# Kernel tuning notes

Hardware: AMD Instinct MI355X
Metric: run time of the kernel (lower is better)

Reference implementation:

```python
import jax, jax.numpy as jnp
import numpy as np

B, D, L, H = 8, 512, 2048, 8
DH = D // H
NEG = -1e30


def setup_inputs() -> dict:
    key = jax.random.key(0)
    k1, k2, k3, k4 = jax.random.split(key, 4)
    queries = jax.random.normal(k1, (B, D, L), dtype=jnp.float32)
    mask = jax.random.randint(k2, (B, L), 0, 2, dtype=jnp.int32)
    w_mem = jax.random.normal(k3, (2 * D, D), dtype=jnp.float32) * (1.0 / np.sqrt(D))
    w_q = jax.random.normal(k4, (D, D), dtype=jnp.float32) * (1.0 / np.sqrt(D))
    return {"queries": queries, "mask": mask, "w_mem": w_mem, "w_q": w_q}


def reference(queries, mask, w_mem, w_q):
    # 1x1 conv == pointwise GEMM over channel dim. queries: [B, D, L]
    memory = jnp.einsum('od,bdl->blo', w_mem, queries)  # [B, L, 2D]
    query = jnp.einsum('od,bdl->blo', w_q, queries)     # [B, L, D]

    def split_heads(x):  # [B, L, C] -> [B, H, L, C/H]
        b, l, c = x.shape
        return x.reshape(b, l, H, c // H).transpose(0, 2, 1, 3)

    k, v = memory[..., :D], memory[..., D:]
    Q = split_heads(query) * (DH ** -0.5)  # [B, H, L, DH]
    K = split_heads(k)
    V = split_heads(v)

    logits = jnp.einsum('bhqd,bhkd->bhqk', Q, K)  # [B, H, L, L]
    m = mask.astype(jnp.float32)[:, None, None, :]  # [B, 1, 1, L]
    logits = logits * m + (1.0 - m) * NEG
    weights = jax.nn.softmax(logits, axis=-1)
    x = jnp.einsum('bhqk,bhkd->bhqd', weights, V)  # [B, H, L, DH]
    # combine heads -> [B, L, D] -> transpose back to [B, D, L]
    out = x.transpose(0, 2, 1, 3).reshape(B, L, D).transpose(0, 2, 1)
    return out
```

## Files before the change

kernel.cpp:

```cpp
#include <hip/hip_runtime.h>
#include <hip/hip_bf16.h>

#define NB 8
#define ND 512
#define NL 2048
#define NH 8
#define NDH 64
#define VROWS 72

typedef __attribute__((ext_vector_type(8))) short bf16x8;
typedef __attribute__((ext_vector_type(4))) float f32x4;
typedef __attribute__((ext_vector_type(4))) unsigned int u32x4;

__device__ __forceinline__ unsigned short f2bf(float x) {
    return (unsigned short)((__float_as_uint(x) + 0x8000u) >> 16);
}

__device__ __forceinline__ float exp2_fast(float x) {
#if __has_builtin(__builtin_amdgcn_exp2f)
    return __builtin_amdgcn_exp2f(x);
#else
    return exp2f(x);
#endif
}

__device__ __forceinline__ unsigned int pack_bf16(float a, float b) {
#if __has_builtin(__builtin_amdgcn_cvt_pk_bf16_f32)
    auto r = __builtin_amdgcn_cvt_pk_bf16_f32(a, b);
    unsigned int u;
    __builtin_memcpy(&u, &r, 4);
    return u;
#else
    unsigned int ua = __float_as_uint(a) + 0x8000u;
    unsigned int ub = __float_as_uint(b) + 0x8000u;
    return __builtin_amdgcn_perm(ub, ua, 0x07060302u);
#endif
}

__device__ __forceinline__ int perm64(int k) {
    return (k & 32) | ((k & 12) << 1) | ((k & 16) >> 2) | (k & 3);
}

__device__ __forceinline__ void async16(void* lds, const void* g) {
    __builtin_amdgcn_global_load_lds(
        (const __attribute__((address_space(1))) unsigned int*)g,
        (__attribute__((address_space(3))) unsigned int*)lds, 16, 0, 0);
}

__global__ __launch_bounds__(256) void prep(
    const float* __restrict__ qin,
    const float* __restrict__ w_mem, const float* __restrict__ w_q,
    const int* __restrict__ maskp,
    unsigned short* __restrict__ Xt, unsigned short* __restrict__ Wc,
    unsigned short* __restrict__ Vt, unsigned short* __restrict__ Kh,
    int* __restrict__ cmap, int* __restrict__ ntile)
{
    const int bid = blockIdx.x;
    const int t = threadIdx.x;
    if (bid < 2048) {
        __shared__ __align__(16) unsigned short T[64][72];
        const int l0 = (bid & 31) * 64, d0 = ((bid >> 5) & 7) * 64, b = bid >> 8;
        const float* X = qin + ((size_t)b * ND + d0) * NL + l0;
        #pragma unroll
        for (int i = 0; i < 4; ++i) {
            int e = t + i * 256;
            int d = e >> 4, l4 = (e & 15) * 4;
            float4 v = *(const float4*)(X + (size_t)d * NL + l4);
            T[l4 + 0][d] = f2bf(v.x);
            T[l4 + 1][d] = f2bf(v.y);
            T[l4 + 2][d] = f2bf(v.z);
            T[l4 + 3][d] = f2bf(v.w);
        }
        __syncthreads();
        #pragma unroll
        for (int i = 0; i < 2; ++i) {
            int e = t + i * 256;
            int row = e >> 3, c8 = (e & 7) * 8;
            *(bf16x8*)(Xt + ((size_t)b * NL + l0 + row) * ND + d0 + c8) =
                *(const bf16x8*)&T[row][c8];
        }
    } else if (bid < 2432) {
        int idx = ((bid - 2048) * 256 + t) * 8;
        int o = idx >> 9, k = idx & 511;
        const float* src;
        float sc;
        if (o < 1024) { src = w_mem + (size_t)o * ND + k; sc = 1.0f; }
        else          { src = w_q + (size_t)(o - 1024) * ND + k;
                        sc = 0.125f * 1.4426950408889634f; }
        float4 f0 = *(const float4*)src;
        float4 f1 = *(const float4*)(src + 4);
        ushort4 p0 = { f2bf(f0.x * sc), f2bf(f0.y * sc), f2bf(f0.z * sc), f2bf(f0.w * sc) };
        ushort4 p1 = { f2bf(f1.x * sc), f2bf(f1.y * sc), f2bf(f1.z * sc), f2bf(f1.w * sc) };
        *(ushort4*)(Wc + idx) = p0;
        *(ushort4*)(Wc + idx + 4) = p1;
    } else {
        __shared__ int wsum[4];
        const int b = bid - 2432;
        const int lane = t & 63, wv = t >> 6;
        int4 ma = *(const int4*)&maskp[b * NL + t * 8];
        int4 mb = *(const int4*)&maskp[b * NL + t * 8 + 4];
        int m[8] = {ma.x, ma.y, ma.z, ma.w, mb.x, mb.y, mb.z, mb.w};
        int loc = 0;
        #pragma unroll
        for (int i = 0; i < 8; ++i) loc += m[i];
        int sc = loc;
        #pragma unroll
        for (int off = 1; off < 64; off <<= 1) {
            int v = __shfl_up(sc, off);
            if (lane >= off) sc += v;
        }
        if (lane == 63) wsum[wv] = sc;
        __syncthreads();
        int wbase = 0;
        #pragma unroll
        for (int i = 0; i < 4; ++i) if (i < wv) wbase += wsum[i];
        int j = wbase + sc - loc;
        #pragma unroll
        for (int i = 0; i < 8; ++i) {
            cmap[b * NL + t * 8 + i] = m[i] ? j : -1;
            j += m[i];
        }
        const int nb = wsum[0] + wsum[1] + wsum[2] + wsum[3];
        const int Nt = (nb + 63) & ~63;
        if (t == 0) ntile[b] = Nt >> 6;
        const int pad = Nt - nb;
        for (int h = 0; h < NH; ++h) {
            unsigned short* row64 = Vt + (((size_t)(b * NH + h)) * VROWS + 64) * NL;
            for (int jj = t; jj < Nt; jj += 256)
                row64[(jj & ~63) | perm64(jj & 63)] =
                    (jj < nb) ? (unsigned short)0x3F80 : (unsigned short)0;
            for (int e = t; e < pad * 64; e += 256) {
                int jj = nb + (e >> 6), dd = e & 63;
                int slot = (jj & ~63) | perm64(jj & 63);
                Vt[(((size_t)(b * NH + h)) * VROWS + dd) * NL + slot] = 0;
                Kh[(((size_t)(b * NH + h)) * NL + jj) * NDH + dd] = 0;
            }
        }
    }
}

__global__ __launch_bounds__(256, 3) void proj_mfma(
    const unsigned short* __restrict__ Wc,
    const unsigned short* __restrict__ Xt,
    const int* __restrict__ cmap,
    unsigned short* __restrict__ Kh,
    unsigned short* __restrict__ Qh,
    unsigned short* __restrict__ Vt)
{
    __shared__ __align__(16) unsigned short As[128 * 64];
    __shared__ __align__(16) unsigned short Bs[128 * 64];

    const int b  = blockIdx.z;
    const int m0 = blockIdx.y * 128;
    const int n0 = blockIdx.x * 128;
    const int t  = threadIdx.x;
    const int w = t >> 6, lane = t & 63, quad = lane >> 4, lq = lane & 15;
    const int wo = (w >> 1) * 64, wl = (w & 1) * 64;
    const int lr = lane >> 3;
    const int cbsw = (lane & 7) ^ lr;
    const bool isV = (m0 >= 512) && (m0 < 1024);
    const f32x4 z4 = {0.f, 0.f, 0.f, 0.f};
    const int sw[2] = {(quad ^ (lq & 7)) * 8, ((4 + quad) ^ (lq & 7)) * 8};

    f32x4 acc[4][4];
    #pragma unroll
    for (int im = 0; im < 4; ++im)
        #pragma unroll
        for (int in = 0; in < 4; ++in) acc[im][in] = z4;

    if (!isV) {
        for (int k0 = 0; k0 < ND; k0 += 64) {
            __syncthreads();
            #pragma unroll 2
            for (int i = w; i < 32; i += 4) {
                if (i < 16) {
                    int R = i * 8;
                    async16(&As[R * 64],
                            Wc + (size_t)(m0 + R + lr) * ND + k0 + cbsw * 8);
                } else {
                    int R = (i - 16) * 8;
                    async16(&Bs[R * 64],
                            Xt + ((size_t)b * NL + n0 + R + lr) * ND + k0 + cbsw * 8);
                }
            }
            __syncthreads();
            #pragma unroll
            for (int ks = 0; ks < 2; ++ks) {
                bf16x8 af[4], bfr[4];
                #pragma unroll
                for (int im = 0; im < 4; ++im)
                    af[im] = *(const bf16x8*)&As[(wo + im * 16 + lq) * 64 + sw[ks]];
                #pragma unroll
                for (int in = 0; in < 4; ++in)
                    bfr[in] = *(const bf16x8*)&Bs[(wl + in * 16 + lq) * 64 + sw[ks]];
                #pragma unroll
                for (int im = 0; im < 4; ++im)
                    #pragma unroll
                    for (int in = 0; in < 4; ++in)
                        acc[im][in] = __builtin_amdgcn_mfma_f32_16x16x32_bf16(
                            af[im], bfr[in], acc[im][in], 0, 0, 0);
            }
        }
        if (m0 < 512) {
            int j[4];
            #pragma unroll
            for (int in = 0; in < 4; ++in)
                j[in] = cmap[b * NL + n0 + wl + in * 16 + lq];
            #pragma unroll
            for (int im = 0; im < 4; ++im) {
                int o  = (m0 + wo + im * 16 + quad * 4) & 511;
                int hh = o >> 6, dh = o & 63;
                #pragma unroll
                for (int in = 0; in < 4; ++in) {
                    if (j[in] >= 0) {
                        ushort4 pk = { f2bf(acc[im][in][0]), f2bf(acc[im][in][1]),
                                       f2bf(acc[im][in][2]), f2bf(acc[im][in][3]) };
                        *(ushort4*)&Kh[(((size_t)b * NH + hh) * NL + j[in]) * NDH + dh] = pk;
                    }
                }
            }
        } else {
            #pragma unroll
            for (int im = 0; im < 4; ++im) {
                int o  = (m0 + wo + im * 16 + quad * 4) & 511;
                int hh = o >> 6, dh = o & 63;
                #pragma unroll
                for (int in = 0; in < 4; ++in) {
                    int l = n0 + wl + in * 16 + lq;
                    ushort4 pk = { f2bf(acc[im][in][0]), f2bf(acc[im][in][1]),
                                   f2bf(acc[im][in][2]), f2bf(acc[im][in][3]) };
                    *(ushort4*)&Qh[(((size_t)b * NH + hh) * NL + l) * NDH + dh] = pk;
                }
            }
        }
    } else {
        for (int k0 = 0; k0 < ND; k0 += 64) {
            __syncthreads();
            #pragma unroll 2
            for (int i = w; i < 32; i += 4) {
                if (i < 16) {
                    int R = i * 8;
                    async16(&As[R * 64],
                            Wc + (size_t)(m0 + R + lr) * ND + k0 + cbsw * 8);
                } else {
                    int R = (i - 16) * 8;
                    async16(&Bs[R * 64],
                            Xt + ((size_t)b * NL + n0 + R + lr) * ND + k0 + cbsw * 8);
                }
            }
            __syncthreads();
            #pragma unroll
            for (int ks = 0; ks < 2; ++ks) {
                bf16x8 af[4], bfr[4];
                #pragma unroll
                for (int im = 0; im < 4; ++im)
                    af[im] = *(const bf16x8*)&As[(wo + im * 16 + lq) * 64 + sw[ks]];
                #pragma unroll
                for (int in = 0; in < 4; ++in)
                    bfr[in] = *(const bf16x8*)&Bs[(wl + in * 16 + lq) * 64 + sw[ks]];
                #pragma unroll
                for (int im = 0; im < 4; ++im)
                    #pragma unroll
                    for (int in = 0; in < 4; ++in)
                        acc[im][in] = __builtin_amdgcn_mfma_f32_16x16x32_bf16(
                            bfr[im], af[in], acc[im][in], 0, 0, 0);
            }
        }
        #pragma unroll
        for (int im = 0; im < 4; ++im) {
            int l4 = n0 + wl + im * 16 + quad * 4;
            int4 j4 = *(const int4*)&cmap[b * NL + l4];
            int jj[4] = {j4.x, j4.y, j4.z, j4.w};
            int slot[4];
            #pragma unroll
            for (int r = 0; r < 4; ++r)
                slot[r] = (jj[r] & ~63) | perm64(jj[r] & 63);
            #pragma unroll
            for (int in = 0; in < 4; ++in) {
                int o  = m0 - 512 + wo + in * 16 + lq;
                int hh = o >> 6, dd = o & 63;
                const size_t rowbase = (((size_t)(b * NH + hh)) * VROWS + dd) * NL;
                #pragma unroll
                for (int r = 0; r < 4; ++r)
                    if (jj[r] >= 0)
                        Vt[rowbase + slot[r]] = f2bf(acc[im][in][r]);
            }
        }
    }
}

__global__ __launch_bounds__(512, 4) void attn_mfma(
    const unsigned short* __restrict__ Qh,
    const unsigned short* __restrict__ Kh,
    const unsigned short* __restrict__ Vt,
    const int* __restrict__ ntilep,
    float* __restrict__ out)
{
    __shared__ __align__(16) unsigned short Ks2[2][64 * 64];
    __shared__ __align__(16) unsigned short Vs2[2][80 * 64];

    const int id = blockIdx.x;
    const int h  = id & 7;
    const int b  = (id >> 3) & 7;
    const int q0 = (id >> 6) * 256;
    const int t = threadIdx.x;
    const int w = t >> 6;
    const int lane = t & 63, quad = lane >> 4, lq = lane & 15;
    const int lr = lane >> 3;
    const int cbsw = (lane & 7) ^ lr;
    const f32x4 z4 = {0.f, 0.f, 0.f, 0.f};

    const unsigned short* Qg = Qh + ((size_t)(b * NH + h)) * NL * NDH;
    const unsigned short* Kg = Kh + ((size_t)(b * NH + h)) * NL * NDH;
    const unsigned short* Vg = Vt + ((size_t)(b * NH + h)) * VROWS * NL;
    const int ntiles = ntilep[b];

    const int sw0 = (quad ^ (lq & 7)) * 8;
    const int sw1 = ((4 + quad) ^ (lq & 7)) * 8;

    const unsigned short* kgp = Kg + (size_t)(w * 8 + lr) * NDH + cbsw * 8;
    const unsigned short* vgp = Vg + (size_t)(w * 8 + lr) * NL + cbsw * 8;
    const unsigned short* vgm = Vg + (size_t)(64 + lr) * NL + cbsw * 8;

    auto stage = [&](unsigned short* Kd, unsigned short* Vd, int kn) {
        async16(Kd + w * 512, kgp + (size_t)kn * NDH);
        async16(Vd + w * 512, vgp + kn);
        if (w == 7) async16(Vd + 8 * 512, vgm + kn);
    };

    stage(Ks2[0], Vs2[0], 0);

    bf16x8 qf[2][2];
    #pragma unroll
    for (int ni = 0; ni < 2; ++ni)
        #pragma unroll
        for (int ks = 0; ks < 2; ++ks)
            qf[ni][ks] = *(const bf16x8*)
                &Qg[(size_t)(q0 + w * 32 + ni * 16 + lq) * NDH + ks * 32 + quad * 8];

    f32x4 oacc[5][2];
    #pragma unroll
    for (int dm = 0; dm < 5; ++dm)
        #pragma unroll
        for (int ni = 0; ni < 2; ++ni) oacc[dm][ni] = z4;

    auto body = [&](const unsigned short* KsB, const unsigned short* VsB,
                    unsigned short* KsN, unsigned short* VsN,
                    int kn, bool pf) {
        __syncthreads();
        if (pf) stage(KsN, VsN, kn);

        const unsigned short* kb0 = KsB + lq * 64 + sw0;
        const unsigned short* kb1 = KsB + lq * 64 + sw1;
        const unsigned short* vb0 = VsB + lq * 64 + sw0;
        const unsigned short* vb1 = VsB + lq * 64 + sw1;

        f32x4 sacc[4][2];
        #pragma unroll
        for (int mi = 0; mi < 4; ++mi) {
            bf16x8 kf = *(const bf16x8*)&kb0[mi * 1024];
            sacc[mi][0] = __builtin_amdgcn_mfma_f32_16x16x32_bf16(kf, qf[0][0], z4, 0, 0, 0);
            sacc[mi][1] = __builtin_amdgcn_mfma_f32_16x16x32_bf16(kf, qf[1][0], z4, 0, 0, 0);
        }
        #pragma unroll
        for (int mi = 0; mi < 4; ++mi) {
            bf16x8 kf = *(const bf16x8*)&kb1[mi * 1024];
            sacc[mi][0] = __builtin_amdgcn_mfma_f32_16x16x32_bf16(kf, qf[0][1], sacc[mi][0], 0, 0, 0);
            sacc[mi][1] = __builtin_amdgcn_mfma_f32_16x16x32_bf16(kf, qf[1][1], sacc[mi][1], 0, 0, 0);
        }

        #pragma unroll
        for (int ks = 0; ks < 2; ++ks) {
            u32x4 pfu[2];
            #pragma unroll
            for (int half = 0; half < 2; ++half) {
                const int mi = ks * 2 + half, jp = half * 2;
                #pragma unroll
                for (int ni = 0; ni < 2; ++ni) {
                    float e0 = exp2_fast(sacc[mi][ni][0]);
                    float e1 = exp2_fast(sacc[mi][ni][1]);
                    float e2 = exp2_fast(sacc[mi][ni][2]);
                    float e3 = exp2_fast(sacc[mi][ni][3]);
                    pfu[ni][jp + 0] = pack_bf16(e0, e1);
                    pfu[ni][jp + 1] = pack_bf16(e2, e3);
                }
            }
            const unsigned short* vb = ks ? vb1 : vb0;
            #pragma unroll
            for (int dm = 0; dm < 5; ++dm) {
                bf16x8 vf = *(const bf16x8*)&vb[dm * 1024];
                oacc[dm][0] = __builtin_amdgcn_mfma_f32_16x16x32_bf16(
                    vf, __builtin_bit_cast(bf16x8, pfu[0]), oacc[dm][0], 0, 0, 0);
                oacc[dm][1] = __builtin_amdgcn_mfma_f32_16x16x32_bf16(
                    vf, __builtin_bit_cast(bf16x8, pfu[1]), oacc[dm][1], 0, 0, 0);
            }
        }
    };

    int kt = 0;
    #pragma unroll 1
    for (; kt + 2 <= ntiles; kt += 2) {
        body(Ks2[0], Vs2[0], Ks2[1], Vs2[1], (kt + 1) * 64, true);
        body(Ks2[1], Vs2[1], Ks2[0], Vs2[0], (kt + 2) * 64, kt + 2 < ntiles);
    }
    if (kt < ntiles)
        body(Ks2[0], Vs2[0], Ks2[1], Vs2[1], 0, false);

    float inv[2];
    #pragma unroll
    for (int ni = 0; ni < 2; ++ni)
        inv[ni] = 1.0f / __shfl(oacc[4][ni][0], lq);

    #pragma unroll
    for (int dm = 0; dm < 4; ++dm)
        #pragma unroll
        for (int ni = 0; ni < 2; ++ni)
            #pragma unroll
            for (int r = 0; r < 4; ++r) {
                int dh = dm * 16 + quad * 4 + r;
                int l  = q0 + w * 32 + ni * 16 + lq;
                out[((size_t)b * ND + h * NDH + dh) * NL + l] =
                    oacc[dm][ni][r] * inv[ni];
            }
}

extern "C" void kernel_launch(void* const* d_in, const int* in_sizes, int n_in,
                              void* d_out, int out_size, void* d_ws, size_t ws_size,
                              hipStream_t stream) {
    const float* queries = (const float*)d_in[0];
    const int*   maskp   = (const int*)d_in[1];
    const float* w_mem   = (const float*)d_in[2];
    const float* w_q     = (const float*)d_in[3];
    float* out = (float*)d_out;

    const size_t headElems  = (size_t)NB * NH * NL * NDH;
    const size_t vElems     = (size_t)NB * NH * VROWS * NL;
    unsigned short* Kh = (unsigned short*)d_ws;
    unsigned short* Vt = Kh + headElems;
    unsigned short* Qh = Vt + vElems;
    unsigned short* Wc = Qh + headElems;
    unsigned short* Xt = Wc + (size_t)1536 * ND;
    int* cmap  = (int*)(Xt + (size_t)NB * NL * ND);
    int* ntile = cmap + NB * NL;

    prep<<<2440, 256, 0, stream>>>(queries, w_mem, w_q, maskp,
                                   Xt, Wc, Vt, Kh, cmap, ntile);

    dim3 g1(NL / 128, 1536 / 128, NB);
    proj_mfma<<<g1, 256, 0, stream>>>(Wc, Xt, cmap, Kh, Qh, Vt);

    attn_mfma<<<512, 512, 0, stream>>>(Qh, Kh, Vt, ntile, out);
}
```

Baseline: 181.3 us.

## Compute K/V projections only for unmasked positions via gathered index list

Prep now builds a compacted list of valid (mask=1) positions per batch instead of a position-to-compact map. The K and V projection blocks gather input rows through this list and return early for tiles beyond the valid count, so roughly half of the K/V GEMM work is skipped. Stores then go directly to compacted indices, bounded by the valid count. In exchange the B-tile loads become indirect gathers and the output depends on correct zero padding of the index list.

Result: no change. 184.4 us (+1.7%).

```diff
diff --git a/kernel.cpp b/kernel.cpp
--- a/kernel.cpp
+++ b/kernel.cpp
@@ -53,7 +53,7 @@
     const int* __restrict__ maskp,
     unsigned short* __restrict__ Xt, unsigned short* __restrict__ Wc,
     unsigned short* __restrict__ Vt, unsigned short* __restrict__ Kh,
-    int* __restrict__ cmap, int* __restrict__ ntile)
+    int* __restrict__ ilist, int* __restrict__ ntile, int* __restrict__ nvalid)
 {
     const int bid = blockIdx.x;
     const int t = threadIdx.x;
@@ -117,12 +117,14 @@
         int j = wbase + sc - loc;
         #pragma unroll
         for (int i = 0; i < 8; ++i) {
-            cmap[b * NL + t * 8 + i] = m[i] ? j : -1;
+            if (m[i]) ilist[b * NL + j] = t * 8 + i;
             j += m[i];
         }
         const int nb = wsum[0] + wsum[1] + wsum[2] + wsum[3];
         const int Nt = (nb + 63) & ~63;
-        if (t == 0) ntile[b] = Nt >> 6;
+        if (t == 0) { ntile[b] = Nt >> 6; nvalid[b] = nb; }
+        const int Nt2 = (nb + 127) & ~127;
+        for (int e = nb + t; e < Nt2; e += 256) ilist[b * NL + e] = 0;
         const int pad = Nt - nb;
         for (int h = 0; h < NH; ++h) {
             unsigned short* row64 = Vt + (((size_t)(b * NH + h)) * VROWS + 64) * NL;
@@ -142,7 +144,9 @@
 __global__ __launch_bounds__(256, 3) void proj_mfma(
     const unsigned short* __restrict__ Wc,
     const unsigned short* __restrict__ Xt,
-    const int* __restrict__ cmap,
+    const int* __restrict__ ilist,
+    const int* __restrict__ ntilep,
+    const int* __restrict__ nvalidp,
     unsigned short* __restrict__ Kh,
     unsigned short* __restrict__ Qh,
     unsigned short* __restrict__ Vt)
@@ -158,9 +162,25 @@
     const int wo = (w >> 1) * 64, wl = (w & 1) * 64;
     const int lr = lane >> 3;
     const int cbsw = (lane & 7) ^ lr;
-    const bool isV = (m0 >= 512) && (m0 < 1024);
+    const bool isQ = (m0 >= 1024);
+    const bool isV = (m0 >= 512) && !isQ;
     const f32x4 z4 = {0.f, 0.f, 0.f, 0.f};
     const int sw[2] = {(quad ^ (lq & 7)) * 8, ((4 + quad) ^ (lq & 7)) * 8};
+
+    int nb = NL;
+    if (!isQ) {
+        const int Nt = ntilep[b] * 64;
+        if (n0 >= Nt) return;
+        nb = nvalidp[b];
+    }
+
+    const unsigned short* bsrc[4];
+    #pragma unroll
+    for (int jx = 0; jx < 4; ++jx) {
+        int row = n0 + w * 8 + 32 * jx + lr;
+        int l = isQ ? row : ilist[b * NL + row];
+        bsrc[jx] = Xt + ((size_t)b * NL + l) * ND + cbsw * 8;
+    }
 
     f32x4 acc[4][4];
     #pragma unroll
@@ -171,17 +191,16 @@
     if (!isV) {
         for (int k0 = 0; k0 < ND; k0 += 64) {
             __syncthreads();
-            #pragma unroll 2
-            for (int i = w; i < 32; i += 4) {
-                if (i < 16) {
-                    int R = i * 8;
-                    async16(&As[R * 64],
-                            Wc + (size_t)(m0 + R + lr) * ND + k0 + cbsw * 8);
-                } else {
-                    int R = (i - 16) * 8;
-                    async16(&Bs[R * 64],
-                            Xt + ((size_t)b * NL + n0 + R + lr) * ND + k0 + cbsw * 8);
-                }
+            #pragma unroll
+            for (int jx = 0; jx < 4; ++jx) {
+                int R = (w + 4 * jx) * 8;
+                async16(&As[R * 64],
+                        Wc + (size_t)(m0 + R + lr) * ND + k0 + cbsw * 8);
+            }
+            #pragma unroll
+            for (int jx = 0; jx < 4; ++jx) {
+                int R = (w + 4 * jx) * 8;
+                async16(&Bs[R * 64], bsrc[jx] + k0);
             }
             __syncthreads();
             #pragma unroll
@@ -202,20 +221,17 @@
             }
         }
         if (m0 < 512) {
-            int j[4];
-            #pragma unroll
-            for (int in = 0; in < 4; ++in)
-                j[in] = cmap[b * NL + n0 + wl + in * 16 + lq];
             #pragma unroll
             for (int im = 0; im < 4; ++im) {
                 int o  = (m0 + wo + im * 16 + quad * 4) & 511;
                 int hh = o >> 6, dh = o & 63;
                 #pragma unroll
                 for (int in = 0; in < 4; ++in) {
-                    if (j[in] >= 0) {
+                    int j = n0 + wl + in * 16 + lq;
+                    if (j < nb) {
                         ushort4 pk = { f2bf(acc[im][in][0]), f2bf(acc[im][in][1]),
                                        f2bf(acc[im][in][2]), f2bf(acc[im][in][3]) };
-                        *(ushort4*)&Kh[(((size_t)b * NH + hh) * NL + j[in]) * NDH + dh] = pk;
+                        *(ushort4*)&Kh[(((size_t)b * NH + hh) * NL + j) * NDH + dh] = pk;
                     }
                 }
             }
@@ -236,17 +252,16 @@
     } else {
         for (int k0 = 0; k0 < ND; k0 += 64) {
             __syncthreads();
-            #pragma unroll 2
-            for (int i = w; i < 32; i += 4) {
-                if (i < 16) {
-                    int R = i * 8;
-                    async16(&As[R * 64],
-                            Wc + (size_t)(m0 + R + lr) * ND + k0 + cbsw * 8);
-                } else {
-                    int R = (i - 16) * 8;
-                    async16(&Bs[R * 64],
-                            Xt + ((size_t)b * NL + n0 + R + lr) * ND + k0 + cbsw * 8);
-                }
+            #pragma unroll
+            for (int jx = 0; jx < 4; ++jx) {
+                int R = (w + 4 * jx) * 8;
+                async16(&As[R * 64],
+                        Wc + (size_t)(m0 + R + lr) * ND + k0 + cbsw * 8);
+            }
+            #pragma unroll
+            for (int jx = 0; jx < 4; ++jx) {
+                int R = (w + 4 * jx) * 8;
+                async16(&Bs[R * 64], bsrc[jx] + k0);
             }
             __syncthreads();
             #pragma unroll
@@ -268,13 +283,15 @@
         }
         #pragma unroll
         for (int im = 0; im < 4; ++im) {
-            int l4 = n0 + wl + im * 16 + quad * 4;
-            int4 j4 = *(const int4*)&cmap[b * NL + l4];
-            int jj[4] = {j4.x, j4.y, j4.z, j4.w};
+            int j4 = n0 + wl + im * 16 + quad * 4;
             int slot[4];
-            #pragma unroll
-            for (int r = 0; r < 4; ++r)
-                slot[r] = (jj[r] & ~63) | perm64(jj[r] & 63);
+            bool ok[4];
+            #pragma unroll
+            for (int r = 0; r < 4; ++r) {
+                int j = j4 + r;
+                ok[r] = (j < nb);
+                slot[r] = (j & ~63) | perm64(j & 63);
+            }
             #pragma unroll
             for (int in = 0; in < 4; ++in) {
                 int o  = m0 - 512 + wo + in * 16 + lq;
@@ -282,7 +299,7 @@
                 const size_t rowbase = (((size_t)(b * NH + hh)) * VROWS + dd) * NL;
                 #pragma unroll
                 for (int r = 0; r < 4; ++r)
-                    if (jj[r] >= 0)
+                    if (ok[r])
                         Vt[rowbase + slot[r]] = f2bf(acc[im][in][r]);
             }
         }
@@ -440,14 +457,15 @@
     unsigned short* Qh = Vt + vElems;
     unsigned short* Wc = Qh + headElems;
     unsigned short* Xt = Wc + (size_t)1536 * ND;
-    int* cmap  = (int*)(Xt + (size_t)NB * NL * ND);
-    int* ntile = cmap + NB * NL;
+    int* ilist  = (int*)(Xt + (size_t)NB * NL * ND);
+    int* ntile  = ilist + NB * NL;
+    int* nvalid = ntile + NB;
 
     prep<<<2440, 256, 0, stream>>>(queries, w_mem, w_q, maskp,
-                                   Xt, Wc, Vt, Kh, cmap, ntile);
+                                   Xt, Wc, Vt, Kh, ilist, ntile, nvalid);
 
     dim3 g1(NL / 128, 1536 / 128, NB);
-    proj_mfma<<<g1, 256, 0, stream>>>(Wc, Xt, cmap, Kh, Qh, Vt);
+    proj_mfma<<<g1, 256, 0, stream>>>(Wc, Xt, ilist, ntile, nvalid, Kh, Qh, Vt);
 
     attn_mfma<<<512, 512, 0, stream>>>(Qh, Kh, Vt, ntile, out);
 }
```

## Double-buffer projection GEMM LDS tiles with a single barrier per k-step

Applied to the files above, without the earlier changes.

Restructures the projection GEMM mainloop to use two 32-wide K tiles in LDS. The next tile's async global-to-LDS loads are issued while MFMAs run on the current tile, so each k-step needs one barrier instead of two. It adds a new XOR swizzle for the narrower rows and raises the launch-bounds occupancy hint from 3 to 4 blocks. The risk is more loop iterations and tighter register limits, possibly causing spills, while the attention kernel likely still dominates total time.

Measured after the change: 185.5 us. +2.3%, slower.

```diff
diff --git a/kernel.cpp b/kernel.cpp
--- a/kernel.cpp
+++ b/kernel.cpp
@@ -139,7 +139,7 @@
     }
 }
 
-__global__ __launch_bounds__(256, 3) void proj_mfma(
+__global__ __launch_bounds__(256, 4) void proj_mfma(
     const unsigned short* __restrict__ Wc,
     const unsigned short* __restrict__ Xt,
     const int* __restrict__ cmap,
@@ -147,8 +147,8 @@
     unsigned short* __restrict__ Qh,
     unsigned short* __restrict__ Vt)
 {
-    __shared__ __align__(16) unsigned short As[128 * 64];
-    __shared__ __align__(16) unsigned short Bs[128 * 64];
+    __shared__ __align__(16) unsigned short As[2][128 * 32];
+    __shared__ __align__(16) unsigned short Bs[2][128 * 32];
 
     const int b  = blockIdx.z;
     const int m0 = blockIdx.y * 128;
@@ -156,11 +156,32 @@
     const int t  = threadIdx.x;
     const int w = t >> 6, lane = t & 63, quad = lane >> 4, lq = lane & 15;
     const int wo = (w >> 1) * 64, wl = (w & 1) * 64;
-    const int lr = lane >> 3;
-    const int cbsw = (lane & 7) ^ lr;
     const bool isV = (m0 >= 512) && (m0 < 1024);
     const f32x4 z4 = {0.f, 0.f, 0.f, 0.f};
-    const int sw[2] = {(quad ^ (lq & 7)) * 8, ((4 + quad) ^ (lq & 7)) * 8};
+
+    const int srow = lane >> 2, schunk = lane & 3;
+    const int r0s = w * 32 + srow, r1s = r0s + 16;
+    const int gc0 = (schunk ^ ((r0s & 3) ^ ((r0s >> 2) & 3))) * 8;
+    const int gc1 = (schunk ^ ((r1s & 3) ^ ((r1s >> 2) & 3))) * 8;
+    const unsigned short* aA0 = Wc + (size_t)(m0 + r0s) * ND + gc0;
+    const unsigned short* aA1 = Wc + (size_t)(m0 + r1s) * ND + gc1;
+    const unsigned short* aB0 = Xt + ((size_t)b * NL + n0 + r0s) * ND + gc0;
+    const unsigned short* aB1 = Xt + ((size_t)b * NL + n0 + r1s) * ND + gc1;
+
+    auto stage = [&](int pb, int k0) {
+        async16(&As[pb][(w * 32) * 32],      aA0 + k0);
+        async16(&As[pb][(w * 32 + 16) * 32], aA1 + k0);
+        async16(&Bs[pb][(w * 32) * 32],      aB0 + k0);
+        async16(&Bs[pb][(w * 32 + 16) * 32], aB1 + k0);
+    };
+    auto lda = [&](int pb, int r) -> bf16x8 {
+        int x = (r & 3) ^ ((r >> 2) & 3);
+        return *(const bf16x8*)&As[pb][r * 32 + (quad ^ x) * 8];
+    };
+    auto ldb = [&](int pb, int r) -> bf16x8 {
+        int x = (r & 3) ^ ((r >> 2) & 3);
+        return *(const bf16x8*)&Bs[pb][r * 32 + (quad ^ x) * 8];
+    };
 
     f32x4 acc[4][4];
     #pragma unroll
@@ -168,38 +189,24 @@
         #pragma unroll
         for (int in = 0; in < 4; ++in) acc[im][in] = z4;
 
+    stage(0, 0);
     if (!isV) {
-        for (int k0 = 0; k0 < ND; k0 += 64) {
+        #pragma unroll 2
+        for (int kk = 0; kk < 16; ++kk) {
+            const int pb = kk & 1;
             __syncthreads();
-            #pragma unroll 2
-            for (int i = w; i < 32; i += 4) {
-                if (i < 16) {
-                    int R = i * 8;
-                    async16(&As[R * 64],
-                            Wc + (size_t)(m0 + R + lr) * ND + k0 + cbsw * 8);
-                } else {
-                    int R = (i - 16) * 8;
-                    async16(&Bs[R * 64],
-                            Xt + ((size_t)b * NL + n0 + R + lr) * ND + k0 + cbsw * 8);
-                }
-            }
-            __syncthreads();
-            #pragma unroll
-            for (int ks = 0; ks < 2; ++ks) {
-                bf16x8 af[4], bfr[4];
-                #pragma unroll
-                for (int im = 0; im < 4; ++im)
-                    af[im] = *(const bf16x8*)&As[(wo + im * 16 + lq) * 64 + sw[ks]];
+            if (kk < 15) stage(pb ^ 1, (kk + 1) * 32);
+            bf16x8 af[4], bfr[4];
+            #pragma unroll
+            for (int im = 0; im < 4; ++im) af[im] = lda(pb, wo + im * 16 + lq);
+            #pragma unroll
+            for (int in = 0; in < 4; ++in) bfr[in] = ldb(pb, wl + in * 16 + lq);
+            #pragma unroll
+            for (int im = 0; im < 4; ++im)
                 #pragma unroll
                 for (int in = 0; in < 4; ++in)
-                    bfr[in] = *(const bf16x8*)&Bs[(wl + in * 16 + lq) * 64 + sw[ks]];
-                #pragma unroll
-                for (int im = 0; im < 4; ++im)
-                    #pragma unroll
-                    for (int in = 0; in < 4; ++in)
-                        acc[im][in] = __builtin_amdgcn_mfma_f32_16x16x32_bf16(
-                            af[im], bfr[in], acc[im][in], 0, 0, 0);
-            }
+                    acc[im][in] = __builtin_amdgcn_mfma_f32_16x16x32_bf16(
+                        af[im], bfr[in], acc[im][in], 0, 0, 0);
         }
         if (m0 < 512) {
             int j[4];
@@ -234,37 +241,22 @@
             }
         }
     } else {
-        for (int k0 = 0; k0 < ND; k0 += 64) {
+        #pragma unroll 2
+        for (int kk = 0; kk < 16; ++kk) {
+            const int pb = kk & 1;
             __syncthreads();
-            #pragma unroll 2
-            for (int i = w; i < 32; i += 4) {
-                if (i < 16) {
-                    int R = i * 8;
-                    async16(&As[R * 64],
-                            Wc + (size_t)(m0 + R + lr) * ND + k0 + cbsw * 8);
-                } else {
-                    int R = (i - 16) * 8;
-                    async16(&Bs[R * 64],
-                            Xt + ((size_t)b * NL + n0 + R + lr) * ND + k0 + cbsw * 8);
-                }
-            }
-            __syncthreads();
-            #pragma unroll
-            for (int ks = 0; ks < 2; ++ks) {
-                bf16x8 af[4], bfr[4];
-                #pragma unroll
-                for (int im = 0; im < 4; ++im)
-                    af[im] = *(const bf16x8*)&As[(wo + im * 16 + lq) * 64 + sw[ks]];
+            if (kk < 15) stage(pb ^ 1, (kk + 1) * 32);
+            bf16x8 af[4], bfr[4];
+            #pragma unroll
+            for (int im = 0; im < 4; ++im) af[im] = lda(pb, wo + im * 16 + lq);
+            #pragma unroll
+            for (int in = 0; in < 4; ++in) bfr[in] = ldb(pb, wl + in * 16 + lq);
+            #pragma unroll
+            for (int im = 0; im < 4; ++im)
                 #pragma unroll
                 for (int in = 0; in < 4; ++in)
-                    bfr[in] = *(const bf16x8*)&Bs[(wl + in * 16 + lq) * 64 + sw[ks]];
-                #pragma unroll
-                for (int im = 0; im < 4; ++im)
-                    #pragma unroll
-                    for (int in = 0; in < 4; ++in)
-                        acc[im][in] = __builtin_amdgcn_mfma_f32_16x16x32_bf16(
-                            bfr[im], af[in], acc[im][in], 0, 0, 0);
-            }
+                    acc[im][in] = __builtin_amdgcn_mfma_f32_16x16x32_bf16(
+                        bfr[im], af[in], acc[im][in], 0, 0, 0);
         }
         #pragma unroll
         for (int im = 0; im < 4; ++im) {
```

## Compute softmax denominator from packed probabilities instead of ones-row MFMA

Applied to the files above, without the earlier changes.

Removes the extra ones-row in the transposed V matrix that was used to get the softmax row sum through a fifth MFMA tile. The attention kernel now sums the bf16-packed exponentials in registers, reduces them across lanes, and subtracts the padded-key count, which needs a new nvalid array. It also spreads the mask-compaction padding work across one block per (batch, head) instead of looping over heads in one block. This saves MFMA work, LDS and V loads in the hot loop, at the cost of extra VALU adds per tile.

Measured after the change: 174.7 us. -3.6%, faster.

```diff
diff --git a/kernel.cpp b/kernel.cpp
--- a/kernel.cpp
+++ b/kernel.cpp
@@ -53,7 +53,7 @@
     const int* __restrict__ maskp,
     unsigned short* __restrict__ Xt, unsigned short* __restrict__ Wc,
     unsigned short* __restrict__ Vt, unsigned short* __restrict__ Kh,
-    int* __restrict__ cmap, int* __restrict__ ntile)
+    int* __restrict__ cmap, int* __restrict__ ntile, int* __restrict__ nvalid)
 {
     const int bid = blockIdx.x;
     const int t = threadIdx.x;
@@ -95,7 +95,8 @@
         *(ushort4*)(Wc + idx + 4) = p1;
     } else {
         __shared__ int wsum[4];
-        const int b = bid - 2432;
+        const int sb = bid - 2432;
+        const int b = sb >> 3, hh = sb & 7;
         const int lane = t & 63, wv = t >> 6;
         int4 ma = *(const int4*)&maskp[b * NL + t * 8];
         int4 mb = *(const int4*)&maskp[b * NL + t * 8 + 4];
@@ -115,26 +116,23 @@
         #pragma unroll
         for (int i = 0; i < 4; ++i) if (i < wv) wbase += wsum[i];
         int j = wbase + sc - loc;
-        #pragma unroll
-        for (int i = 0; i < 8; ++i) {
-            cmap[b * NL + t * 8 + i] = m[i] ? j : -1;
-            j += m[i];
+        if (hh == 0) {
+            int jj = j;
+            #pragma unroll
+            for (int i = 0; i < 8; ++i) {
+                cmap[b * NL + t * 8 + i] = m[i] ? jj : -1;
+                jj += m[i];
+            }
         }
         const int nb = wsum[0] + wsum[1] + wsum[2] + wsum[3];
         const int Nt = (nb + 63) & ~63;
-        if (t == 0) ntile[b] = Nt >> 6;
+        if (hh == 0 && t == 0) { ntile[b] = Nt >> 6; nvalid[b] = nb; }
         const int pad = Nt - nb;
-        for (int h = 0; h < NH; ++h) {
-            unsigned short* row64 = Vt + (((size_t)(b * NH + h)) * VROWS + 64) * NL;
-            for (int jj = t; jj < Nt; jj += 256)
-                row64[(jj & ~63) | perm64(jj & 63)] =
-                    (jj < nb) ? (unsigned short)0x3F80 : (unsigned short)0;
-            for (int e = t; e < pad * 64; e += 256) {
-                int jj = nb + (e >> 6), dd = e & 63;
-                int slot = (jj & ~63) | perm64(jj & 63);
-                Vt[(((size_t)(b * NH + h)) * VROWS + dd) * NL + slot] = 0;
-                Kh[(((size_t)(b * NH + h)) * NL + jj) * NDH + dd] = 0;
-            }
+        for (int e = t; e < pad * 64; e += 256) {
+            int jj = nb + (e >> 6), dd = e & 63;
+            int slot = (jj & ~63) | perm64(jj & 63);
+            Vt[(((size_t)(b * NH + hh)) * VROWS + dd) * NL + slot] = 0;
+            Kh[(((size_t)(b * NH + hh)) * NL + jj) * NDH + dd] = 0;
         }
     }
 }
@@ -294,10 +292,11 @@
     const unsigned short* __restrict__ Kh,
     const unsigned short* __restrict__ Vt,
     const int* __restrict__ ntilep,
+    const int* __restrict__ nvalidp,
     float* __restrict__ out)
 {
     __shared__ __align__(16) unsigned short Ks2[2][64 * 64];
-    __shared__ __align__(16) unsigned short Vs2[2][80 * 64];
+    __shared__ __align__(16) unsigned short Vs2[2][64 * 64];
 
     const int id = blockIdx.x;
     const int h  = id & 7;
@@ -320,12 +319,10 @@
 
     const unsigned short* kgp = Kg + (size_t)(w * 8 + lr) * NDH + cbsw * 8;
     const unsigned short* vgp = Vg + (size_t)(w * 8 + lr) * NL + cbsw * 8;
-    const unsigned short* vgm = Vg + (size_t)(64 + lr) * NL + cbsw * 8;
 
     auto stage = [&](unsigned short* Kd, unsigned short* Vd, int kn) {
         async16(Kd + w * 512, kgp + (size_t)kn * NDH);
         async16(Vd + w * 512, vgp + kn);
-        if (w == 7) async16(Vd + 8 * 512, vgm + kn);
     };
 
     stage(Ks2[0], Vs2[0], 0);
@@ -338,11 +335,12 @@
             qf[ni][ks] = *(const bf16x8*)
                 &Qg[(size_t)(q0 + w * 32 + ni * 16 + lq) * NDH + ks * 32 + quad * 8];
 
-    f32x4 oacc[5][2];
+    f32x4 oacc[4][2];
     #pragma unroll
-    for (int dm = 0; dm < 5; ++dm)
+    for (int dm = 0; dm < 4; ++dm)
         #pragma unroll
         for (int ni = 0; ni < 2; ++ni) oacc[dm][ni] = z4;
+    float ls[2] = {0.f, 0.f};
 
     auto body = [&](const unsigned short* KsB, const unsigned short* VsB,
                     unsigned short* KsN, unsigned short* VsN,
@@ -387,13 +385,21 @@
             }
             const unsigned short* vb = ks ? vb1 : vb0;
             #pragma unroll
-            for (int dm = 0; dm < 5; ++dm) {
+            for (int dm = 0; dm < 4; ++dm) {
                 bf16x8 vf = *(const bf16x8*)&vb[dm * 1024];
                 oacc[dm][0] = __builtin_amdgcn_mfma_f32_16x16x32_bf16(
                     vf, __builtin_bit_cast(bf16x8, pfu[0]), oacc[dm][0], 0, 0, 0);
                 oacc[dm][1] = __builtin_amdgcn_mfma_f32_16x16x32_bf16(
                     vf, __builtin_bit_cast(bf16x8, pfu[1]), oacc[dm][1], 0, 0, 0);
             }
+            #pragma unroll
+            for (int ni = 0; ni < 2; ++ni)
+                #pragma unroll
+                for (int jw = 0; jw < 4; ++jw) {
+                    unsigned int u = pfu[ni][jw];
+                    ls[ni] += __uint_as_float(u << 16);
+                    ls[ni] += __uint_as_float(u & 0xFFFF0000u);
+                }
         }
     };
 
@@ -406,10 +412,15 @@
     if (kt < ntiles)
         body(Ks2[0], Vs2[0], Ks2[1], Vs2[1], 0, false);
 
+    const float padc = (float)(ntiles * 64 - nvalidp[b]);
     float inv[2];
     #pragma unroll
-    for (int ni = 0; ni < 2; ++ni)
-        inv[ni] = 1.0f / __shfl(oacc[4][ni][0], lq);
+    for (int ni = 0; ni < 2; ++ni) {
+        float s = ls[ni];
+        s += __shfl_xor(s, 16);
+        s += __shfl_xor(s, 32);
+        inv[ni] = 1.0f / (s - padc);
+    }
 
     #pragma unroll
     for (int dm = 0; dm < 4; ++dm)
@@ -440,14 +451,15 @@
     unsigned short* Qh = Vt + vElems;
     unsigned short* Wc = Qh + headElems;
     unsigned short* Xt = Wc + (size_t)1536 * ND;
-    int* cmap  = (int*)(Xt + (size_t)NB * NL * ND);
-    int* ntile = cmap + NB * NL;
-
-    prep<<<2440, 256, 0, stream>>>(queries, w_mem, w_q, maskp,
-                                   Xt, Wc, Vt, Kh, cmap, ntile);
+    int* cmap   = (int*)(Xt + (size_t)NB * NL * ND);
+    int* ntile  = cmap + NB * NL;
+    int* nvalid = ntile + NB;
+
+    prep<<<2496, 256, 0, stream>>>(queries, w_mem, w_q, maskp,
+                                   Xt, Wc, Vt, Kh, cmap, ntile, nvalid);
 
     dim3 g1(NL / 128, 1536 / 128, NB);
     proj_mfma<<<g1, 256, 0, stream>>>(Wc, Xt, cmap, Kh, Qh, Vt);
 
-    attn_mfma<<<512, 512, 0, stream>>>(Qh, Kh, Vt, ntile, out);
-}
+    attn_mfma<<<512, 512, 0, stream>>>(Qh, Kh, Vt, ntile, nvalid, out);
+}
```
